# Kernel tuning notes

Hardware: AMD Instinct MI355X
Metric: run time of the kernel (lower is better)

The kernel has to match this reference:

```python
import jax, jax.numpy as jnp
import numpy as np

NUM_NODES = 1_000_000
EMBED_DIM = 64
N_BATCH = 8192
DEG = 32


def setup_inputs() -> dict:
    key = jax.random.key(0)
    k_feat, k_alpha, k_nodes, k1, k2, k3 = jax.random.split(key, 6)
    features = jax.random.normal(k_feat, (NUM_NODES, EMBED_DIM), dtype=jnp.float32)
    # xavier-uniform-ish init for alpha (2*embed_dim, 3)
    alpha = jax.random.normal(k_alpha, (2 * EMBED_DIM, 3), dtype=jnp.float32)
    nodes = jax.random.randint(k_nodes, (N_BATCH,), 0, NUM_NODES, dtype=jnp.int32)
    neigh_idx1 = jax.random.randint(k1, (N_BATCH, DEG), 0, NUM_NODES, dtype=jnp.int32)
    neigh_idx2 = jax.random.randint(k2, (N_BATCH, DEG), 0, NUM_NODES, dtype=jnp.int32)
    neigh_idx3 = jax.random.randint(k3, (N_BATCH, DEG), 0, NUM_NODES, dtype=jnp.int32)
    return {
        "features": features,
        "alpha": alpha,
        "nodes": nodes,
        "neigh_idx1": neigh_idx1,
        "neigh_idx2": neigh_idx2,
        "neigh_idx3": neigh_idx3,
    }


def reference(features, alpha, nodes, neigh_idx1, neigh_idx2, neigh_idx3):
    # self features for the batch nodes: (n, d)
    self_feats = features[nodes]

    def intra(nidx):
        # mean aggregation of neighbor embeddings (FRAUDRE IntraAgg):
        # gather (n, deg, d) -> mean over deg -> (n, d)
        agg = features[nidx].mean(axis=1)
        # concat self || agg, then ReLU -> (n, 2d)
        return jax.nn.relu(jnp.concatenate([self_feats, agg], axis=1))

    r1 = intra(neigh_idx1)
    r2 = intra(neigh_idx2)
    r3 = intra(neigh_idx3)

    # weight_inter_agg: per-feature softmax over the 3 relations
    w = jax.nn.softmax(alpha, axis=1)              # (2d, 3)
    stacked = jnp.stack([r1, r2, r3], axis=-1)     # (n, 2d, 3)
    aggregated = jnp.einsum('ndr,dr->nd', stacked, w)  # (n, 2d)

    # final: self_feats || inter-aggregated -> (n, 3d)
    return jnp.concatenate([self_feats, aggregated], axis=1)
```

## Files before the change

kernel.cpp:

```cpp
#include <hip/hip_runtime.h>
#include <hip/hip_bf16.h>

#define EMBED 64
#define DEG 32

__global__ __launch_bounds__(256) void interagg_kernel(
    const float* __restrict__ features,
    const float* __restrict__ alpha,
    const int* __restrict__ nodes,
    const int* __restrict__ ni1,
    const int* __restrict__ ni2,
    const int* __restrict__ ni3,
    float* __restrict__ out)
{
    __shared__ float s_self[EMBED];
    __shared__ float s_w[3][EMBED];
    __shared__ float s_agg[3][EMBED];

    const int n    = blockIdx.x;
    const int tid  = threadIdx.x;
    const int wave = tid >> 6;
    const int lane = tid & 63;

    if (wave < 3) {
        const int* nb = ((wave == 0) ? ni1 : (wave == 1) ? ni2 : ni3) + n * DEG;
        const int g   = lane >> 4;
        const int sub = lane & 15;

        int idx[8];
        #pragma unroll
        for (int k = 0; k < 8; k++) idx[k] = nb[g + 4 * k];

        const float4* f4 = (const float4*)features;
        float acc0 = 0.f, acc1 = 0.f, acc2 = 0.f, acc3 = 0.f;
        #pragma unroll
        for (int k = 0; k < 8; k++) {
            float4 v = f4[(size_t)idx[k] * 16 + sub];
            acc0 += v.x; acc1 += v.y; acc2 += v.z; acc3 += v.w;
        }

        #pragma unroll
        for (int off = 16; off < 64; off <<= 1) {
            acc0 += __shfl_xor(acc0, off, 64);
            acc1 += __shfl_xor(acc1, off, 64);
            acc2 += __shfl_xor(acc2, off, 64);
            acc3 += __shfl_xor(acc3, off, 64);
        }

        if (g == 0) {
            float m0 = acc0 * (1.0f / DEG);
            float m1 = acc1 * (1.0f / DEG);
            float m2 = acc2 * (1.0f / DEG);
            float m3 = acc3 * (1.0f / DEG);
            s_agg[wave][sub * 4 + 0] = m0 > 0.f ? m0 : 0.f;
            s_agg[wave][sub * 4 + 1] = m1 > 0.f ? m1 : 0.f;
            s_agg[wave][sub * 4 + 2] = m2 > 0.f ? m2 : 0.f;
            s_agg[wave][sub * 4 + 3] = m3 > 0.f ? m3 : 0.f;
        }
    } else {
        const int node = nodes[n];
        s_self[lane] = features[(size_t)node * EMBED + lane];

        const int row = 64 + lane;
        float a0 = alpha[row * 3 + 0];
        float a1 = alpha[row * 3 + 1];
        float a2 = alpha[row * 3 + 2];
        float mx = fmaxf(a0, fmaxf(a1, a2));
        float e0 = expf(a0 - mx), e1 = expf(a1 - mx), e2 = expf(a2 - mx);
        float inv = 1.0f / (e0 + e1 + e2);
        s_w[0][lane] = e0 * inv;
        s_w[1][lane] = e1 * inv;
        s_w[2][lane] = e2 * inv;
    }

    __syncthreads();

    const size_t base = (size_t)n * 192;
    if (tid < 64) {
        out[base + tid] = s_self[tid];
    } else if (tid < 128) {
        const int j = tid - 64;
        float v = s_self[j];
        out[base + tid] = v > 0.f ? v : 0.f;
    } else if (tid < 192) {
        const int j = tid - 128;
        out[base + tid] = s_agg[0][j] * s_w[0][j]
                        + s_agg[1][j] * s_w[1][j]
                        + s_agg[2][j] * s_w[2][j];
    }
}

extern "C" void kernel_launch(void* const* d_in, const int* in_sizes, int n_in,
                              void* d_out, int out_size, void* d_ws, size_t ws_size,
                              hipStream_t stream) {
    const float* features = (const float*)d_in[0];
    const float* alpha    = (const float*)d_in[1];
    const int* nodes      = (const int*)d_in[2];
    const int* ni1        = (const int*)d_in[3];
    const int* ni2        = (const int*)d_in[4];
    const int* ni3        = (const int*)d_in[5];
    float* out            = (float*)d_out;

    const int nbatch = in_sizes[2];
    interagg_kernel<<<nbatch, 256, 0, stream>>>(
        features, alpha, nodes, ni1, ni2, ni3, out);
}
```

Baseline: 329.4 us.

## Process one batch node per wave, removing shared memory and block barrier

Each wave now handles a whole batch node: it gathers all three relations' neighbor rows, the self row and the softmax weights in registers. The results are redistributed with shuffles instead of shared memory and __syncthreads. Each block covers four nodes, so the grid shrinks fourfold and every wave stays busy through the output phase. In exchange each wave keeps 24 gathers in flight and uses more registers, and the relation-select shuffles add some ALU work.

```diff
diff --git a/kernel.cpp b/kernel.cpp
--- a/kernel.cpp
+++ b/kernel.cpp
@@ -1,5 +1,4 @@
 #include <hip/hip_runtime.h>
-#include <hip/hip_bf16.h>
 
 #define EMBED 64
 #define DEG 32
@@ -11,83 +10,85 @@
     const int* __restrict__ ni1,
     const int* __restrict__ ni2,
     const int* __restrict__ ni3,
-    float* __restrict__ out)
+    float* __restrict__ out,
+    int nbatch)
 {
-    __shared__ float s_self[EMBED];
-    __shared__ float s_w[3][EMBED];
-    __shared__ float s_agg[3][EMBED];
-
-    const int n    = blockIdx.x;
     const int tid  = threadIdx.x;
     const int wave = tid >> 6;
     const int lane = tid & 63;
+    const int n    = blockIdx.x * 4 + wave;
+    if (n >= nbatch) return;
 
-    if (wave < 3) {
-        const int* nb = ((wave == 0) ? ni1 : (wave == 1) ? ni2 : ni3) + n * DEG;
-        const int g   = lane >> 4;
-        const int sub = lane & 15;
+    const int g   = lane >> 4;
+    const int sub = lane & 15;
 
-        int idx[8];
+    const int* nb0 = ni1 + (size_t)n * DEG;
+    const int* nb1 = ni2 + (size_t)n * DEG;
+    const int* nb2 = ni3 + (size_t)n * DEG;
+    const float4* f4 = (const float4*)features;
+
+    int idx[3][8];
+    #pragma unroll
+    for (int k = 0; k < 8; k++) {
+        idx[0][k] = nb0[g + 4 * k];
+        idx[1][k] = nb1[g + 4 * k];
+        idx[2][k] = nb2[g + 4 * k];
+    }
+
+    const int node = nodes[n];
+    const float self_v = features[(size_t)node * EMBED + lane];
+    const int arow = 64 + lane;
+    const float a0 = alpha[arow * 3 + 0];
+    const float a1 = alpha[arow * 3 + 1];
+    const float a2 = alpha[arow * 3 + 2];
+
+    float acc[3][4];
+    #pragma unroll
+    for (int r = 0; r < 3; r++)
         #pragma unroll
-        for (int k = 0; k < 8; k++) idx[k] = nb[g + 4 * k];
+        for (int e = 0; e < 4; e++) acc[r][e] = 0.f;
 
-        const float4* f4 = (const float4*)features;
-        float acc0 = 0.f, acc1 = 0.f, acc2 = 0.f, acc3 = 0.f;
+    #pragma unroll
+    for (int r = 0; r < 3; r++) {
         #pragma unroll
         for (int k = 0; k < 8; k++) {
-            float4 v = f4[(size_t)idx[k] * 16 + sub];
-            acc0 += v.x; acc1 += v.y; acc2 += v.z; acc3 += v.w;
+            float4 v = f4[(size_t)idx[r][k] * 16 + sub];
+            acc[r][0] += v.x; acc[r][1] += v.y;
+            acc[r][2] += v.z; acc[r][3] += v.w;
+        }
+    }
+
+    #pragma unroll
+    for (int r = 0; r < 3; r++)
+        #pragma unroll
+        for (int e = 0; e < 4; e++) {
+            acc[r][e] += __shfl_xor(acc[r][e], 16, 64);
+            acc[r][e] += __shfl_xor(acc[r][e], 32, 64);
         }
 
-        #pragma unroll
-        for (int off = 16; off < 64; off <<= 1) {
-            acc0 += __shfl_xor(acc0, off, 64);
-            acc1 += __shfl_xor(acc1, off, 64);
-            acc2 += __shfl_xor(acc2, off, 64);
-            acc3 += __shfl_xor(acc3, off, 64);
-        }
-
-        if (g == 0) {
-            float m0 = acc0 * (1.0f / DEG);
-            float m1 = acc1 * (1.0f / DEG);
-            float m2 = acc2 * (1.0f / DEG);
-            float m3 = acc3 * (1.0f / DEG);
-            s_agg[wave][sub * 4 + 0] = m0 > 0.f ? m0 : 0.f;
-            s_agg[wave][sub * 4 + 1] = m1 > 0.f ? m1 : 0.f;
-            s_agg[wave][sub * 4 + 2] = m2 > 0.f ? m2 : 0.f;
-            s_agg[wave][sub * 4 + 3] = m3 > 0.f ? m3 : 0.f;
-        }
-    } else {
-        const int node = nodes[n];
-        s_self[lane] = features[(size_t)node * EMBED + lane];
-
-        const int row = 64 + lane;
-        float a0 = alpha[row * 3 + 0];
-        float a1 = alpha[row * 3 + 1];
-        float a2 = alpha[row * 3 + 2];
-        float mx = fmaxf(a0, fmaxf(a1, a2));
-        float e0 = expf(a0 - mx), e1 = expf(a1 - mx), e2 = expf(a2 - mx);
-        float inv = 1.0f / (e0 + e1 + e2);
-        s_w[0][lane] = e0 * inv;
-        s_w[1][lane] = e1 * inv;
-        s_w[2][lane] = e2 * inv;
+    const int src   = lane >> 2;
+    const int e_sel = lane & 3;
+    float relagg[3];
+    #pragma unroll
+    for (int r = 0; r < 3; r++) {
+        float t0 = __shfl(acc[r][0], src, 64);
+        float t1 = __shfl(acc[r][1], src, 64);
+        float t2 = __shfl(acc[r][2], src, 64);
+        float t3 = __shfl(acc[r][3], src, 64);
+        float t  = (e_sel == 0) ? t0 : (e_sel == 1) ? t1 : (e_sel == 2) ? t2 : t3;
+        t *= (1.0f / DEG);
+        relagg[r] = t > 0.f ? t : 0.f;
     }
 
-    __syncthreads();
+    const float mx  = fmaxf(a0, fmaxf(a1, a2));
+    const float e0  = __expf(a0 - mx), e1 = __expf(a1 - mx), e2 = __expf(a2 - mx);
+    const float inv = 1.0f / (e0 + e1 + e2);
 
     const size_t base = (size_t)n * 192;
-    if (tid < 64) {
-        out[base + tid] = s_self[tid];
-    } else if (tid < 128) {
-        const int j = tid - 64;
-        float v = s_self[j];
-        out[base + tid] = v > 0.f ? v : 0.f;
-    } else if (tid < 192) {
-        const int j = tid - 128;
-        out[base + tid] = s_agg[0][j] * s_w[0][j]
-                        + s_agg[1][j] * s_w[1][j]
-                        + s_agg[2][j] * s_w[2][j];
-    }
+    out[base + lane] = self_v;
+    out[base + 64 + lane] = self_v > 0.f ? self_v : 0.f;
+    out[base + 128 + lane] =
+        (relagg[0] * e0 + relagg[1] * e1 + relagg[2] * e2) * inv;
 }
 
 extern "C" void kernel_launch(void* const* d_in, const int* in_sizes, int n_in,
@@ -102,6 +103,7 @@
     float* out            = (float*)d_out;
 
     const int nbatch = in_sizes[2];
-    interagg_kernel<<<nbatch, 256, 0, stream>>>(
-        features, alpha, nodes, ni1, ni2, ni3, out);
+    const int blocks = (nbatch + 3) / 4;
+    interagg_kernel<<<blocks, 256, 0, stream>>>(
+        features, alpha, nodes, ni1, ni2, ni3, out, nbatch);
 }
```

Measured after the change: 328.3 us. Within noise of the previous version (-0.3%).
